# Kernel optimization log

Measured on AMD Instinct MI355X. Metric: run time of the kernel, lower is better.

The kernel has to match this reference:

```python
import jax, jax.numpy as jnp
import numpy as np

N, E, IN, H, C, G = 50000, 1600000, 128, 4, 32, 64  # nodes, edges, in_ch, heads, hidden, graphs
OUT = 1
NEG_SLOPE = 0.2


def setup_inputs() -> dict:
    key = jax.random.key(0)
    ks = jax.random.split(key, 16)
    d = {
        "x": jax.random.normal(ks[0], (N, IN), dtype=jnp.float32),
        "edge_index": jax.random.randint(ks[1], (2, E), 0, N, dtype=jnp.int64),
        "batch": jnp.sort(jax.random.randint(ks[2], (N,), 0, G, dtype=jnp.int64)),
    }
    s = 1.0 / np.sqrt(IN)
    # layer 0: in=IN, layer 1: in=H*C (=128)
    d["W0"] = jax.random.normal(ks[3], (IN, H * C), dtype=jnp.float32) * s
    d["a_src0"] = jax.random.normal(ks[4], (H, C), dtype=jnp.float32) * s
    d["a_dst0"] = jax.random.normal(ks[5], (H, C), dtype=jnp.float32) * s
    d["b0"] = jnp.zeros((H * C,), dtype=jnp.float32)
    d["W1"] = jax.random.normal(ks[6], (H * C, H * C), dtype=jnp.float32) * s
    d["a_src1"] = jax.random.normal(ks[7], (H, C), dtype=jnp.float32) * s
    d["a_dst1"] = jax.random.normal(ks[8], (H, C), dtype=jnp.float32) * s
    d["b1"] = jnp.zeros((H * C,), dtype=jnp.float32)
    d["lin_w"] = jax.random.normal(ks[9], (H * C, OUT), dtype=jnp.float32) * s
    d["lin_b"] = jnp.zeros((OUT,), dtype=jnp.float32)
    return d


def gat_conv(x, src, dst, W, a_src, a_dst, b):
    # x: [N, F_in]; src/dst: [E'] (self-loops already appended, PyG default)
    n = x.shape[0]
    xw = (x @ W).reshape(n, H, C)                      # [N, H, C]
    alpha_s = jnp.sum(xw * a_src, axis=-1)             # [N, H]
    alpha_d = jnp.sum(xw * a_dst, axis=-1)             # [N, H]
    e = jax.nn.leaky_relu(alpha_s[src] + alpha_d[dst], NEG_SLOPE)  # [E', H]
    # segment softmax over edges grouped by destination node
    m = jax.ops.segment_max(e, dst, num_segments=n)    # [N, H]
    ex = jnp.exp(e - m[dst])
    denom = jax.ops.segment_sum(ex, dst, num_segments=n)
    alpha = ex / denom[dst]                            # [E', H]
    msg = xw[src] * alpha[:, :, None]                  # [E', H, C]
    out = jax.ops.segment_sum(msg, dst, num_segments=n)
    return out.reshape(n, H * C) + b


def reference(x, edge_index, batch, W0, a_src0, a_dst0, b0, W1, a_src1, a_dst1, b1, lin_w, lin_b):
    loop = jnp.arange(N, dtype=edge_index.dtype)
    src = jnp.concatenate([edge_index[0], loop])
    dst = jnp.concatenate([edge_index[1], loop])
    h = gat_conv(x.astype(jnp.float32), src, dst, W0, a_src0, a_dst0, b0)
    h = jax.nn.elu(h)  # dropout is identity in eval mode
    h = gat_conv(h, src, dst, W1, a_src1, a_dst1, b1)
    h = jax.nn.elu(h)
    # global_mean_pool
    sums = jax.ops.segment_sum(h, batch, num_segments=G)          # [G, H*C]
    cnts = jax.ops.segment_sum(jnp.ones((N,), h.dtype), batch, num_segments=G)
    pooled = sums / jnp.maximum(cnts, 1.0)[:, None]
    return (pooled @ lin_w + lin_b).squeeze()                     # [G]
```

## Files before the change

### kernel.cpp

```cpp
#include <hip/hip_runtime.h>
#include <hip/hip_bf16.h>

#define NN 50000
#define EE 1600000
#define NEDGE (EE + NN)
#define HH 4
#define HC 128
#define GG 64
#define GMT 64
#define NBKT 196
#define BCAP 12544
#define BKE 2048
#define NB1 ((EE + BKE - 1) / BKE)

__device__ __forceinline__ float lrelu(float x) { return x > 0.f ? x : 0.2f * x; }

__device__ __forceinline__ unsigned packbf2(float a, float b) {
    unsigned ua = __float_as_uint(a);
    ua = (ua + 0x7fffu + ((ua >> 16) & 1u)) >> 16;
    unsigned ub = __float_as_uint(b);
    ub = (ub + 0x7fffu + ((ub >> 16) & 1u)) >> 16;
    return ua | (ub << 16);
}

__global__ __launch_bounds__(256) void binit(int* __restrict__ bcur) {
    int t = blockIdx.x * 256 + threadIdx.x;
    if (t < NBKT) bcur[t] = t * BCAP;
}

__global__ __launch_bounds__(256) void bucketize(const int* __restrict__ ei,
                                                 int* __restrict__ bcur,
                                                 uint2* __restrict__ pairs) {
    __shared__ int cnt[NBKT], off[NBKT], rc[NBKT], gbase[NBKT];
    __shared__ int wsum[4], woff[4];
    __shared__ uint2 stage[BKE];
    int t = threadIdx.x;
    int e0 = blockIdx.x * BKE;
    int n = EE - e0; if (n > BKE) n = BKE;
    for (int i = t; i < NBKT; i += 256) cnt[i] = 0;
    __syncthreads();
    unsigned dv[8], sv[8];
#pragma unroll
    for (int k = 0; k < 8; ++k) {
        int i = t + k * 256;
        if (i < n) {
            dv[k] = (unsigned)ei[EE + e0 + i];
            sv[k] = (unsigned)ei[e0 + i];
            atomicAdd(&cnt[dv[k] >> 8], 1);
        }
    }
    __syncthreads();
    {
        int v = (t < NBKT) ? cnt[t] : 0;
        int lane = t & 63, wv = t >> 6;
        int x = v;
#pragma unroll
        for (int o = 1; o < 64; o <<= 1) { int y = __shfl_up(x, o); if (lane >= o) x += y; }
        if (lane == 63) wsum[wv] = x;
        __syncthreads();
        if (t == 0) { int r = 0; for (int k2 = 0; k2 < 4; ++k2) { woff[k2] = r; r += wsum[k2]; } }
        __syncthreads();
        if (t < NBKT) { int e = x - v + woff[wv]; off[t] = e; rc[t] = e; }
    }
    __syncthreads();
#pragma unroll
    for (int k = 0; k < 8; ++k) {
        int i = t + k * 256;
        if (i < n) {
            int b = dv[k] >> 8;
            int p = atomicAdd(&rc[b], 1);
            stage[p] = make_uint2(dv[k], sv[k]);
        }
    }
    __syncthreads();
    if (t < NBKT) { int c = cnt[t]; gbase[t] = c ? atomicAdd(&bcur[t], c) : 0; }
    __syncthreads();
    for (int i = t; i < n; i += 256) {
        uint2 pr = stage[i];
        int b = (int)(pr.x >> 8);
        pairs[(size_t)gbase[b] + (i - off[b])] = pr;
    }
}

__global__ __launch_bounds__(256) void bscan(const int* __restrict__ bcur,
                                             int* __restrict__ bbase) {
    int t = threadIdx.x;
    int v = 0;
    if (t < NBKT) {
        int pcnt = bcur[t] - t * BCAP;
        int nodes = NN - t * 256; if (nodes > 256) nodes = 256;
        v = pcnt + nodes;
    }
    int lane = t & 63, wv = t >> 6;
    int x = v;
#pragma unroll
    for (int o = 1; o < 64; o <<= 1) { int y = __shfl_up(x, o); if (lane >= o) x += y; }
    __shared__ int wsum[4], woff[4];
    if (lane == 63) wsum[wv] = x;
    __syncthreads();
    if (t == 0) { int r = 0; for (int k = 0; k < 4; ++k) { woff[k] = r; r += wsum[k]; } }
    __syncthreads();
    if (t < NBKT) bbase[t] = x - v + woff[wv];
}

__global__ __launch_bounds__(512) void debucket(const uint2* __restrict__ pairs,
                                                const int* __restrict__ bcur,
                                                const int* __restrict__ bbase,
                                                int* __restrict__ row_start,
                                                int* __restrict__ esrc) {
    __shared__ int cnt[256], off[256], cur[256];
    __shared__ int wsum[4], woff[4];
    __shared__ int stage[BCAP + 256];
    int b = blockIdx.x, t = threadIdx.x;
    int n0 = b * 256;
    int nnode = NN - n0; if (nnode > 256) nnode = 256;
    int pcnt = bcur[b] - b * BCAP;
    int base = bbase[b];
    if (t < 256) cnt[t] = 0;
    __syncthreads();
    for (int i = t; i < pcnt; i += 512)
        atomicAdd(&cnt[pairs[(size_t)b * BCAP + i].x & 255u], 1);
    __syncthreads();
    {
        int v = 0, x = 0;
        int lane = t & 63, wv = t >> 6;
        if (t < 256) {
            v = cnt[t] + (t < nnode ? 1 : 0);
            x = v;
#pragma unroll
            for (int o = 1; o < 64; o <<= 1) { int y = __shfl_up(x, o); if (lane >= o) x += y; }
            if (lane == 63) wsum[wv] = x;
        }
        __syncthreads();
        if (t == 0) { int r = 0; for (int k = 0; k < 4; ++k) { woff[k] = r; r += wsum[k]; } }
        __syncthreads();
        if (t < 256) off[t] = x - v + woff[wv];
    }
    __syncthreads();
    if (t < nnode) {
        int o = off[t];
        stage[o] = n0 + t;
        cur[t] = o + 1;
        row_start[n0 + t] = base + o;
    }
    __syncthreads();
    for (int i = t; i < pcnt; i += 512) {
        uint2 pr = pairs[(size_t)b * BCAP + i];
        int p = atomicAdd(&cur[pr.x & 255u], 1);
        stage[p] = (int)pr.y;
    }
    __syncthreads();
    int tot = pcnt + nnode;
    for (int i = t; i < tot; i += 512) esrc[base + i] = stage[i];
    if (b == NBKT - 1 && t == 0) row_start[NN] = NEDGE;
}

__global__ __launch_bounds__(256) void gemm_alpha(
    const float* __restrict__ X, const float* __restrict__ W,
    const float* __restrict__ a_src, const float* __restrict__ a_dst,
    unsigned* __restrict__ xwb, float* __restrict__ as_, float* __restrict__ ad_) {
    __shared__ float xs[GMT][HC + 4];
    int tid = threadIdx.x;
    int n0 = blockIdx.x * GMT;
    for (int i = tid; i < GMT * (HC / 4); i += 256) {
        int r = i >> 5, c4 = i & 31;
        int n = n0 + r;
        float4 v = (n < NN) ? ((const float4*)X)[(size_t)n * 32 + c4]
                            : make_float4(0.f, 0.f, 0.f, 0.f);
        *(float4*)&xs[r][c4 * 4] = v;
    }
    __syncthreads();

    int jg = tid & 31;
    int ng = tid >> 5;
    float4 acc[8] = {};
    for (int k = 0; k < HC; k += 4) {
        float4 wr[4];
#pragma unroll
        for (int dk = 0; dk < 4; ++dk) wr[dk] = ((const float4*)W)[(k + dk) * 32 + jg];
#pragma unroll
        for (int r = 0; r < 8; ++r) {
            float4 xv = *(const float4*)&xs[ng * 8 + r][k];
            acc[r].x = fmaf(xv.x, wr[0].x, acc[r].x);
            acc[r].y = fmaf(xv.x, wr[0].y, acc[r].y);
            acc[r].z = fmaf(xv.x, wr[0].z, acc[r].z);
            acc[r].w = fmaf(xv.x, wr[0].w, acc[r].w);
            acc[r].x = fmaf(xv.y, wr[1].x, acc[r].x);
            acc[r].y = fmaf(xv.y, wr[1].y, acc[r].y);
            acc[r].z = fmaf(xv.y, wr[1].z, acc[r].z);
            acc[r].w = fmaf(xv.y, wr[1].w, acc[r].w);
            acc[r].x = fmaf(xv.z, wr[2].x, acc[r].x);
            acc[r].y = fmaf(xv.z, wr[2].y, acc[r].y);
            acc[r].z = fmaf(xv.z, wr[2].z, acc[r].z);
            acc[r].w = fmaf(xv.z, wr[2].w, acc[r].w);
            acc[r].x = fmaf(xv.w, wr[3].x, acc[r].x);
            acc[r].y = fmaf(xv.w, wr[3].y, acc[r].y);
            acc[r].z = fmaf(xv.w, wr[3].z, acc[r].z);
            acc[r].w = fmaf(xv.w, wr[3].w, acc[r].w);
        }
    }
    float4 asv = ((const float4*)a_src)[jg];
    float4 adv = ((const float4*)a_dst)[jg];
#pragma unroll
    for (int r = 0; r < 8; ++r) {
        int n = n0 + ng * 8 + r;
        float ps = acc[r].x * asv.x + acc[r].y * asv.y + acc[r].z * asv.z + acc[r].w * asv.w;
        float pd = acc[r].x * adv.x + acc[r].y * adv.y + acc[r].z * adv.z + acc[r].w * adv.w;
        ps += __shfl_xor(ps, 1); pd += __shfl_xor(pd, 1);
        ps += __shfl_xor(ps, 2); pd += __shfl_xor(pd, 2);
        ps += __shfl_xor(ps, 4); pd += __shfl_xor(pd, 4);
        if (n < NN) {
            ((uint2*)xwb)[(size_t)n * 32 + jg] =
                make_uint2(packbf2(acc[r].x, acc[r].y), packbf2(acc[r].z, acc[r].w));
            if ((jg & 7) == 0) {
                int h = jg >> 3;
                as_[n * HH + h] = ps;
                ad_[n * HH + h] = pd;
            }
        }
    }
}

#define SWSTR 66
__global__ __launch_bounds__(256) void aggregate(
    const int* __restrict__ esrc, const int* __restrict__ row_start,
    const float* __restrict__ as_, const float* __restrict__ ad_,
    const unsigned* __restrict__ xwb, const float* __restrict__ bias,
    float* __restrict__ out) {
    __shared__ float2 sw_all[4][4 * SWSTR];
    int wid = (int)(threadIdx.x >> 6);
    int node = blockIdx.x * 4 + wid;
    if (node >= NN) return;
    int lane = threadIdx.x & 63;
    float2* sw = &sw_all[wid][0];
    int beg = row_start[node];
    int end = row_start[node + 1];
    float4 ad = ((const float4*)ad_)[node];

    int sub = lane >> 4;
    int c8 = lane & 15;
    int h = c8 >> 2;
    float4 accA = make_float4(0.f, 0.f, 0.f, 0.f);
    float4 accB = make_float4(0.f, 0.f, 0.f, 0.f);
    float d0 = 0.f, d1 = 0.f, d2 = 0.f, d3 = 0.f;

    for (int base = beg; base < end; base += 64) {
        int i = base + lane;
        int cnt = end - base; if (cnt > 64) cnt = 64;
        if (i < end) {
            int s = esrc[i];
            float4 av = ((const float4*)as_)[s];
            float w0 = __expf(lrelu(av.x + ad.x));
            float w1 = __expf(lrelu(av.y + ad.y));
            float w2 = __expf(lrelu(av.z + ad.z));
            float w3 = __expf(lrelu(av.w + ad.w));
            d0 += w0; d1 += w1; d2 += w2; d3 += w3;
            float sf = __int_as_float(s);
            sw[0 * SWSTR + lane] = make_float2(sf, w0);
            sw[1 * SWSTR + lane] = make_float2(sf, w1);
            sw[2 * SWSTR + lane] = make_float2(sf, w2);
            sw[3 * SWSTR + lane] = make_float2(sf, w3);
        }
        int iters = (cnt + 3) >> 2;
#pragma unroll 2
        for (int it = 0; it < iters; ++it) {
            int j = (it << 2) + sub;
            float2 swv = sw[h * SWSTR + j];
            bool ok = j < cnt;
            float wj = ok ? swv.y : 0.f;
            int sj = ok ? __float_as_int(swv.x) : 0;
            uint4 v = ((const uint4*)xwb)[(size_t)sj * 16 + c8];
            accA.x = fmaf(wj, __uint_as_float(v.x << 16), accA.x);
            accA.y = fmaf(wj, __uint_as_float(v.x & 0xffff0000u), accA.y);
            accA.z = fmaf(wj, __uint_as_float(v.y << 16), accA.z);
            accA.w = fmaf(wj, __uint_as_float(v.y & 0xffff0000u), accA.w);
            accB.x = fmaf(wj, __uint_as_float(v.z << 16), accB.x);
            accB.y = fmaf(wj, __uint_as_float(v.z & 0xffff0000u), accB.y);
            accB.z = fmaf(wj, __uint_as_float(v.w << 16), accB.z);
            accB.w = fmaf(wj, __uint_as_float(v.w & 0xffff0000u), accB.w);
        }
    }
#pragma unroll
    for (int off = 16; off <= 32; off <<= 1) {
        accA.x += __shfl_xor(accA.x, off);
        accA.y += __shfl_xor(accA.y, off);
        accA.z += __shfl_xor(accA.z, off);
        accA.w += __shfl_xor(accA.w, off);
        accB.x += __shfl_xor(accB.x, off);
        accB.y += __shfl_xor(accB.y, off);
        accB.z += __shfl_xor(accB.z, off);
        accB.w += __shfl_xor(accB.w, off);
    }
#pragma unroll
    for (int off = 32; off; off >>= 1) {
        d0 += __shfl_xor(d0, off);
        d1 += __shfl_xor(d1, off);
        d2 += __shfl_xor(d2, off);
        d3 += __shfl_xor(d3, off);
    }
    if (sub == 0) {
        float dn = h == 0 ? d0 : (h == 1 ? d1 : (h == 2 ? d2 : d3));
        float inv = 1.f / dn;
        float4 bb0 = ((const float4*)bias)[c8 * 2];
        float4 bb1 = ((const float4*)bias)[c8 * 2 + 1];
        float4 oA, oB;
        oA.x = fmaf(accA.x, inv, bb0.x);
        oA.y = fmaf(accA.y, inv, bb0.y);
        oA.z = fmaf(accA.z, inv, bb0.z);
        oA.w = fmaf(accA.w, inv, bb0.w);
        oB.x = fmaf(accB.x, inv, bb1.x);
        oB.y = fmaf(accB.y, inv, bb1.y);
        oB.z = fmaf(accB.z, inv, bb1.z);
        oB.w = fmaf(accB.w, inv, bb1.w);
        oA.x = oA.x > 0.f ? oA.x : expm1f(oA.x);
        oA.y = oA.y > 0.f ? oA.y : expm1f(oA.y);
        oA.z = oA.z > 0.f ? oA.z : expm1f(oA.z);
        oA.w = oA.w > 0.f ? oA.w : expm1f(oA.w);
        oB.x = oB.x > 0.f ? oB.x : expm1f(oB.x);
        oB.y = oB.y > 0.f ? oB.y : expm1f(oB.y);
        oB.z = oB.z > 0.f ? oB.z : expm1f(oB.z);
        oB.w = oB.w > 0.f ? oB.w : expm1f(oB.w);
        ((float4*)out)[(size_t)node * 32 + c8 * 2] = oA;
        ((float4*)out)[(size_t)node * 32 + c8 * 2 + 1] = oB;
    }
}

__global__ __launch_bounds__(128) void pool(
    const float* __restrict__ h1, const int* __restrict__ batch,
    float* __restrict__ sums, float* __restrict__ cnts) {
    int j = threadIdx.x;
    int n0 = blockIdx.x * 64;
    int n1 = n0 + 64; if (n1 > NN) n1 = NN;
    if (n0 >= NN) return;
    int cur = batch[n0];
    float local = 0.f;
    int cnt = 0;
    for (int n = n0; n < n1; ++n) {
        int g = batch[n];
        if (g != cur) {
            atomicAdd(&sums[cur * HC + j], local);
            if (j == 0) atomicAdd(&cnts[cur], (float)cnt);
            local = 0.f; cnt = 0; cur = g;
        }
        local += h1[(size_t)n * HC + j];
        ++cnt;
    }
    atomicAdd(&sums[cur * HC + j], local);
    if (j == 0) atomicAdd(&cnts[cur], (float)cnt);
}

__global__ __launch_bounds__(128) void head_out(
    const float* __restrict__ sums, const float* __restrict__ cnts,
    const float* __restrict__ lin_w, const float* __restrict__ lin_b,
    float* __restrict__ out) {
    int g = blockIdx.x;
    int j = threadIdx.x;
    float c = cnts[g];
    c = c > 1.f ? c : 1.f;
    float v = sums[g * HC + j] / c * lin_w[j];
    __shared__ float red[HC];
    red[j] = v;
    __syncthreads();
    for (int off = 64; off > 0; off >>= 1) {
        if (j < off) red[j] += red[j + off];
        __syncthreads();
    }
    if (j == 0) out[g] = red[0] + lin_b[0];
}

extern "C" void kernel_launch(void* const* d_in, const int* in_sizes, int n_in,
                              void* d_out, int out_size, void* d_ws, size_t ws_size,
                              hipStream_t stream) {
    const float* x   = (const float*)d_in[0];
    const int*   ei  = (const int*)d_in[1];
    const int*   bat = (const int*)d_in[2];
    const float* W0  = (const float*)d_in[3];
    const float* as0 = (const float*)d_in[4];
    const float* ad0 = (const float*)d_in[5];
    const float* b0  = (const float*)d_in[6];
    const float* W1  = (const float*)d_in[7];
    const float* as1 = (const float*)d_in[8];
    const float* ad1 = (const float*)d_in[9];
    const float* b1  = (const float*)d_in[10];
    const float* lw  = (const float*)d_in[11];
    const float* lb  = (const float*)d_in[12];
    float* out = (float*)d_out;

    char* w = (char*)d_ws;
    unsigned* xwb = (unsigned*)w; w += (size_t)NN * HC * 2;
    float* h0  = (float*)w;  w += (size_t)NN * HC * 4;
    float* as_ = (float*)w;  w += (size_t)NN * HH * 4;
    float* ad_ = (float*)w;  w += (size_t)NN * HH * 4;
    int* row_start = (int*)w; w += (size_t)(NN + 1) * 4;
    int* bcur      = (int*)w; w += (size_t)NBKT * 4;
    int* bbase     = (int*)w; w += (size_t)NBKT * 4;
    int* esrc      = (int*)w; w += (size_t)NEDGE * 4;
    uint2* pairs   = (uint2*)w; w += (size_t)NBKT * BCAP * 8;
    float* sums = (float*)w; w += (size_t)GG * HC * 4;
    float* cnts = (float*)w; w += (size_t)GG * 4;

    const int gb = (NN + GMT - 1) / GMT;
    const int ab = (NN + 3) / 4;

    binit<<<1, 256, 0, stream>>>(bcur);
    bucketize<<<NB1, 256, 0, stream>>>(ei, bcur, pairs);
    bscan<<<1, 256, 0, stream>>>(bcur, bbase);
    debucket<<<NBKT, 512, 0, stream>>>(pairs, bcur, bbase, row_start, esrc);

    gemm_alpha<<<gb, 256, 0, stream>>>(x, W0, as0, ad0, xwb, as_, ad_);
    aggregate<<<ab, 256, 0, stream>>>(esrc, row_start, as_, ad_, xwb, b0, h0);

    gemm_alpha<<<gb, 256, 0, stream>>>(h0, W1, as1, ad1, xwb, as_, ad_);
    aggregate<<<ab, 256, 0, stream>>>(esrc, row_start, as_, ad_, xwb, b1, h0);

    hipMemsetAsync(sums, 0, ((size_t)GG * HC + GG) * 4, stream);
    pool<<<(NN + 63) / 64, 128, 0, stream>>>(h0, bat, sums, cnts);
    head_out<<<GG, 128, 0, stream>>>(sums, cnts, lw, lb, out);
}
```

Before: 263.1 us.

## Store features head-major and split aggregation into one block per head

The xw, alpha_src and alpha_dst buffers move from node-major to head-major layout, and aggregation now launches a separate grid slice per head. Each wavefront handles one node and one head, processing 16 edges at a time with 4 lanes per 64-byte head row. The intent is a smaller per-head gather footprint that fits cache better and less per-edge exp and shared-memory work per wave. In exchange, esrc and row_start are read four times over and there are four times as many blocks.

```diff
diff --git a/kernel.cpp b/kernel.cpp
--- a/kernel.cpp
+++ b/kernel.cpp
@@ -12,8 +12,9 @@
 #define BCAP 12544
 #define BKE 2048
 #define NB1 ((EE + BKE - 1) / BKE)
-
-__device__ __forceinline__ float lrelu(float x) { return x > 0.f ? x : 0.2f * x; }
+#define NPH 12500
+
+__device__ __forceinline__ float lrelu(float x) { return fmaxf(x, 0.2f * x); }
 
 __device__ __forceinline__ unsigned packbf2(float a, float b) {
     unsigned ua = __float_as_uint(a);
@@ -173,6 +174,7 @@
 
     int jg = tid & 31;
     int ng = tid >> 5;
+    int h = jg >> 3;
     float4 acc[8] = {};
     for (int k = 0; k < HC; k += 4) {
         float4 wr[4];
@@ -210,66 +212,58 @@
         ps += __shfl_xor(ps, 2); pd += __shfl_xor(pd, 2);
         ps += __shfl_xor(ps, 4); pd += __shfl_xor(pd, 4);
         if (n < NN) {
-            ((uint2*)xwb)[(size_t)n * 32 + jg] =
+            ((uint2*)xwb)[((size_t)h * NN + n) * 8 + (jg & 7)] =
                 make_uint2(packbf2(acc[r].x, acc[r].y), packbf2(acc[r].z, acc[r].w));
             if ((jg & 7) == 0) {
-                int h = jg >> 3;
-                as_[n * HH + h] = ps;
-                ad_[n * HH + h] = pd;
+                as_[(size_t)h * NN + n] = ps;
+                ad_[(size_t)h * NN + n] = pd;
             }
         }
     }
 }
 
-#define SWSTR 66
 __global__ __launch_bounds__(256) void aggregate(
     const int* __restrict__ esrc, const int* __restrict__ row_start,
     const float* __restrict__ as_, const float* __restrict__ ad_,
     const unsigned* __restrict__ xwb, const float* __restrict__ bias,
     float* __restrict__ out) {
-    __shared__ float2 sw_all[4][4 * SWSTR];
+    __shared__ float2 sw_all[4][68];
+    int bid = blockIdx.x;
+    int hh = bid / NPH;
+    int nb = bid - hh * NPH;
     int wid = (int)(threadIdx.x >> 6);
-    int node = blockIdx.x * 4 + wid;
-    if (node >= NN) return;
+    int node = nb * 4 + wid;
     int lane = threadIdx.x & 63;
-    float2* sw = &sw_all[wid][0];
+    float2* sw = sw_all[wid];
     int beg = row_start[node];
     int end = row_start[node + 1];
-    float4 ad = ((const float4*)ad_)[node];
-
-    int sub = lane >> 4;
-    int c8 = lane & 15;
-    int h = c8 >> 2;
+    const float* ash = as_ + (size_t)hh * NN;
+    float adh = ad_[(size_t)hh * NN + node];
+    int slot = lane >> 2;
+    int le = lane & 3;
+    const char* xwp = (const char*)xwb + ((size_t)hh * NN << 6) + (le << 4);
+
     float4 accA = make_float4(0.f, 0.f, 0.f, 0.f);
     float4 accB = make_float4(0.f, 0.f, 0.f, 0.f);
-    float d0 = 0.f, d1 = 0.f, d2 = 0.f, d3 = 0.f;
+    float dsum = 0.f;
 
     for (int base = beg; base < end; base += 64) {
         int i = base + lane;
         int cnt = end - base; if (cnt > 64) cnt = 64;
         if (i < end) {
             int s = esrc[i];
-            float4 av = ((const float4*)as_)[s];
-            float w0 = __expf(lrelu(av.x + ad.x));
-            float w1 = __expf(lrelu(av.y + ad.y));
-            float w2 = __expf(lrelu(av.z + ad.z));
-            float w3 = __expf(lrelu(av.w + ad.w));
-            d0 += w0; d1 += w1; d2 += w2; d3 += w3;
-            float sf = __int_as_float(s);
-            sw[0 * SWSTR + lane] = make_float2(sf, w0);
-            sw[1 * SWSTR + lane] = make_float2(sf, w1);
-            sw[2 * SWSTR + lane] = make_float2(sf, w2);
-            sw[3 * SWSTR + lane] = make_float2(sf, w3);
-        }
-        int iters = (cnt + 3) >> 2;
-#pragma unroll 2
+            float w = __expf(lrelu(ash[s] + adh));
+            dsum += w;
+            sw[lane] = make_float2(__int_as_float(s), w);
+        }
+        int iters = (cnt + 15) >> 4;
         for (int it = 0; it < iters; ++it) {
-            int j = (it << 2) + sub;
-            float2 swv = sw[h * SWSTR + j];
+            int j = (it << 4) + slot;
             bool ok = j < cnt;
-            float wj = ok ? swv.y : 0.f;
-            int sj = ok ? __float_as_int(swv.x) : 0;
-            uint4 v = ((const uint4*)xwb)[(size_t)sj * 16 + c8];
+            float2 sv = sw[ok ? j : 0];
+            float wj = ok ? sv.y : 0.f;
+            unsigned off = ok ? ((unsigned)__float_as_int(sv.x) << 6) : 0u;
+            uint4 v = *(const uint4*)(xwp + off);
             accA.x = fmaf(wj, __uint_as_float(v.x << 16), accA.x);
             accA.y = fmaf(wj, __uint_as_float(v.x & 0xffff0000u), accA.y);
             accA.z = fmaf(wj, __uint_as_float(v.y << 16), accA.z);
@@ -281,7 +275,7 @@
         }
     }
 #pragma unroll
-    for (int off = 16; off <= 32; off <<= 1) {
+    for (int off = 4; off < 64; off <<= 1) {
         accA.x += __shfl_xor(accA.x, off);
         accA.y += __shfl_xor(accA.y, off);
         accA.z += __shfl_xor(accA.z, off);
@@ -292,17 +286,12 @@
         accB.w += __shfl_xor(accB.w, off);
     }
 #pragma unroll
-    for (int off = 32; off; off >>= 1) {
-        d0 += __shfl_xor(d0, off);
-        d1 += __shfl_xor(d1, off);
-        d2 += __shfl_xor(d2, off);
-        d3 += __shfl_xor(d3, off);
-    }
-    if (sub == 0) {
-        float dn = h == 0 ? d0 : (h == 1 ? d1 : (h == 2 ? d2 : d3));
-        float inv = 1.f / dn;
-        float4 bb0 = ((const float4*)bias)[c8 * 2];
-        float4 bb1 = ((const float4*)bias)[c8 * 2 + 1];
+    for (int off = 32; off; off >>= 1) dsum += __shfl_xor(dsum, off);
+
+    if (lane < 4) {
+        float inv = 1.f / dsum;
+        float4 bb0 = ((const float4*)bias)[hh * 8 + le * 2];
+        float4 bb1 = ((const float4*)bias)[hh * 8 + le * 2 + 1];
         float4 oA, oB;
         oA.x = fmaf(accA.x, inv, bb0.x);
         oA.y = fmaf(accA.y, inv, bb0.y);
@@ -320,8 +309,8 @@
         oB.y = oB.y > 0.f ? oB.y : expm1f(oB.y);
         oB.z = oB.z > 0.f ? oB.z : expm1f(oB.z);
         oB.w = oB.w > 0.f ? oB.w : expm1f(oB.w);
-        ((float4*)out)[(size_t)node * 32 + c8 * 2] = oA;
-        ((float4*)out)[(size_t)node * 32 + c8 * 2 + 1] = oB;
+        ((float4*)out)[(size_t)node * 32 + hh * 8 + le * 2] = oA;
+        ((float4*)out)[(size_t)node * 32 + hh * 8 + le * 2 + 1] = oB;
     }
 }
 
@@ -400,7 +389,7 @@
     float* cnts = (float*)w; w += (size_t)GG * 4;
 
     const int gb = (NN + GMT - 1) / GMT;
-    const int ab = (NN + 3) / 4;
+    const int ab = HH * NPH;
 
     binit<<<1, 256, 0, stream>>>(bcur);
     bucketize<<<NB1, 256, 0, stream>>>(ei, bcur, pairs);
```

Result: slower. 368.8 us (+40.2%).
